# Kernel tuning notes

Measured on AMD Instinct MI355X. Metric: run time of the kernel, lower is better.

The kernel has to match this reference:

```python
import jax, jax.numpy as jnp
import numpy as np

B, S, D = 64, 1024, 128
EPS = 1e-5

def hardswish(x):
    return x * jnp.clip(x + 3.0, 0.0, 6.0) / 6.0

def setup_inputs() -> dict:
    key = jax.random.key(0)
    k1, k2, k3 = jax.random.split(key, 3)
    x = jax.random.normal(k1, (B, S, D), dtype=jnp.float32)
    ln_w = jnp.ones((S, D), dtype=jnp.float32)
    ln_b = jnp.zeros((S, D), dtype=jnp.float32)
    # U1[i]/U2[i] rows packed into lower-triangular (S,S); init ~ N(0,1)*0.01
    W1 = jax.random.normal(k2, (S, S), dtype=jnp.float32) * 0.01
    W2 = jax.random.normal(k3, (S, S), dtype=jnp.float32) * 0.01
    return {"x": x, "ln_w": ln_w, "ln_b": ln_b, "W1": W1, "W2": W2}

def reference(x, ln_w, ln_b, W1, W2):
    # LayerNorm over the last two dims (seq_len, feature_dim) jointly
    mu = jnp.mean(x, axis=(-2, -1), keepdims=True)
    var = jnp.mean(jnp.square(x - mu), axis=(-2, -1), keepdims=True)
    h = (x - mu) * jax.lax.rsqrt(var + EPS) * ln_w + ln_b
    # causal (lower-triangular) time mixing: u[:, t] = sum_{s<=t} W1[t, s] * h[:, s]
    mask = jnp.tril(jnp.ones((S, S), dtype=x.dtype))
    u = hardswish(jnp.einsum('ts,bsd->btd', W1 * mask, h))
    v = jnp.einsum('ts,bsd->btd', W2 * mask, u)
    return x + v
```

## Files before the change

### kernel.cpp

```cpp
#include <hip/hip_runtime.h>
#include <hip/hip_bf16.h>

#define NB 64
#define S_ 1024
#define D_ 128

typedef __attribute__((ext_vector_type(8))) short bf16x8;
typedef __attribute__((ext_vector_type(4))) float f32x4;
typedef __attribute__((ext_vector_type(4))) unsigned int u32x4;


__device__ __forceinline__ unsigned short f2bf(float f) {
  __hip_bfloat16 h = __float2bfloat16(f);
  return __builtin_bit_cast(unsigned short, h);
}

__device__ __forceinline__ void async_copy16(const void* g, void* l) {
  __builtin_amdgcn_global_load_lds(
      (const __attribute__((address_space(1))) unsigned int*)g,
      (__attribute__((address_space(3))) unsigned int*)l, 16, 0, 0);
}

__device__ __forceinline__ void store16_dev(void* p, bf16x8 v) {
  u32x4 d = __builtin_bit_cast(u32x4, v);
  asm volatile("global_store_dwordx4 %0, %1, off sc1" ::"v"(p), "v"(d)
               : "memory");
}

__device__ __forceinline__ void spin_mask(unsigned* p, unsigned need) {
  if (threadIdx.x == 0) {
    int guard = 0;
    while ((__hip_atomic_load(p, __ATOMIC_RELAXED, __HIP_MEMORY_SCOPE_AGENT) &
            need) != need) {
      __builtin_amdgcn_s_sleep(1);
      if (++guard > 2000000) break;
    }
  }
  __syncthreads();
  asm volatile("" ::: "memory");
}

__device__ __forceinline__ void publish_bit(unsigned* p, unsigned bit) {
  asm volatile("s_waitcnt vmcnt(0)" ::: "memory");
  __syncthreads();
  if (threadIdx.x == 0)
    __hip_atomic_fetch_or(p, bit, __ATOMIC_RELAXED, __HIP_MEMORY_SCOPE_AGENT);
}

__global__ __launch_bounds__(256) void wpack_kernel(
    const float* __restrict__ W1, const float* __restrict__ W2,
    unsigned short* __restrict__ W1f, unsigned short* __restrict__ W2f,
    unsigned* __restrict__ stats) {
  const int blk = blockIdx.x;
  const int t = threadIdx.x;
  const int wave = t >> 6, lane = t & 63;
  const int quad = lane >> 4, l16 = lane & 15;
  if (blk == 0) {
#pragma unroll
    for (int i = 0; i < 8; ++i) stats[t + i * 256] = 0u;
  }
#pragma unroll
  for (int rep = 0; rep < 2; ++rep) {
    const int u = blk * 8 + wave * 2 + rep;
    const int f = u & 2047;
    const int p = f >> 5, c = f & 31;
    const int r = p * 16 + l16;
    const int k0 = c * 32 + quad * 8;
    const float* wsrc = ((u >> 11) ? W2 : W1) + (size_t)r * 1024 + k0;
    float4 a0 = ((const float4*)wsrc)[0];
    float4 a1 = ((const float4*)wsrc)[1];
    float av[8] = {a0.x, a0.y, a0.z, a0.w, a1.x, a1.y, a1.z, a1.w};
    bf16x8 o;
#pragma unroll
    for (int jj = 0; jj < 8; ++jj)
      o[jj] = (short)f2bf((k0 + jj <= r) ? av[jj] : 0.f);
    unsigned short* dstp = ((u >> 11) ? W2f : W1f) +
                           ((size_t)p * 32 + c) * 512 + lane * 8;
    *(bf16x8*)dstp = o;
  }
}

template <bool HSWISH>
__device__ __forceinline__ void gemm_phase(
    unsigned short* ldsA, const int b, const int mt, unsigned* flags,
    const unsigned short* __restrict__ Af, const unsigned short* __restrict__ Bf,
    unsigned short* __restrict__ Uf, const float* __restrict__ Xres,
    float* __restrict__ Out) {
  const int t = threadIdx.x;
  const int wave = t >> 6, lane = t & 63;
  const int quad = lane >> 4, l16 = lane & 15;
  const int row0 = mt * 64;

  const int cend = 2 * (mt + 1);
  const int nq = (cend + 3) >> 2;

  const unsigned short* Ab = Af + (size_t)mt * 4 * 32 * 512;
  const unsigned short* Bb = Bf + (size_t)b * (D_ * S_);

  spin_mask(flags, (2u << mt) - 1);

  auto STAGE = [&](int q) {
    unsigned short* buf = ldsA + (q & 1) * 8192;
    const int c0 = q * 4;
    if (wave < cend - c0) {
#pragma unroll
      for (int jc = 0; jc < 4; ++jc) {
        const int flat16 = jc * 256 + t;
        async_copy16(Ab + ((size_t)jc * 32 + c0 + wave) * 512 + lane * 8,
                     buf + flat16 * 8);
      }
    }
  };

  STAGE(0);
  if (nq > 1) STAGE(1);
  __builtin_amdgcn_sched_barrier(0);

  f32x4 acc[4][2] = {};
  bf16x8 Bp[4][2];
#pragma unroll
  for (int g = 0; g < 4; ++g) {
    const int gg = (g < cend) ? g : 0;
#pragma unroll
    for (int jj = 0; jj < 2; ++jj)
      Bp[g][jj] = *(const bf16x8*)(Bb + ((size_t)(wave * 2 + jj) * 32 + gg) * 512 + lane * 8);
  }

  for (int q = 0; q < nq; ++q) {
    if (q < nq - 1)
      asm volatile("s_waitcnt vmcnt(12)" ::: "memory");
    else
      asm volatile("s_waitcnt vmcnt(8)" ::: "memory");
    __builtin_amdgcn_s_barrier();
    __builtin_amdgcn_sched_barrier(0);
    unsigned short* buf = ldsA + (q & 1) * 8192;
#pragma unroll
    for (int c = 0; c < 4; ++c) {
      const int g = q * 4 + c;
      if (g < cend) {
        bf16x8 af[4];
#pragma unroll
        for (int i = 0; i < 4; ++i)
          af[i] = *(const bf16x8*)(buf + i * 2048 + c * 512 + lane * 8);
        __builtin_amdgcn_s_setprio(1);
#pragma unroll
        for (int i = 0; i < 4; ++i)
#pragma unroll
          for (int jj = 0; jj < 2; ++jj)
            acc[i][jj] = __builtin_amdgcn_mfma_f32_16x16x32_bf16(
                af[i], Bp[c][jj], acc[i][jj], 0, 0, 0);
        __builtin_amdgcn_s_setprio(0);
      }
      const int gn = (g + 4 < cend) ? (g + 4) : 0;
#pragma unroll
      for (int jj = 0; jj < 2; ++jj)
        Bp[c][jj] = *(const bf16x8*)(
            Bb + ((size_t)(wave * 2 + jj) * 32 + gn) * 512 + lane * 8);
    }
    __builtin_amdgcn_sched_barrier(0);
    __builtin_amdgcn_s_barrier();
    __builtin_amdgcn_sched_barrier(0);
    if (q + 2 < nq) STAGE(q + 2);
  }

  if (HSWISH) {
    __syncthreads();
    unsigned short* ldsT = ldsA;
#pragma unroll
    for (int i = 0; i < 4; ++i)
#pragma unroll
      for (int jj = 0; jj < 2; ++jj) {
        ushort4 pk;
        float v0 = acc[i][jj][0], v1 = acc[i][jj][1], v2 = acc[i][jj][2], v3 = acc[i][jj][3];
        pk.x = f2bf(v0 * fminf(fmaxf(v0 + 3.f, 0.f), 6.f) * (1.f / 6.f));
        pk.y = f2bf(v1 * fminf(fmaxf(v1 + 3.f, 0.f), 6.f) * (1.f / 6.f));
        pk.z = f2bf(v2 * fminf(fmaxf(v2 + 3.f, 0.f), 6.f) * (1.f / 6.f));
        pk.w = f2bf(v3 * fminf(fmaxf(v3 + 3.f, 0.f), 6.f) * (1.f / 6.f));
        const int n = wave * 32 + jj * 16 + l16;
        const int m0 = i * 16 + quad * 4;
        *(ushort4*)(ldsT + n * 72 + m0) = pk;
      }
    __syncthreads();
    unsigned short* gU = Uf + (size_t)b * (D_ * S_);
#pragma unroll
    for (int ff = 0; ff < 4; ++ff) {
      const int f = wave * 4 + ff;
      const int p2 = f >> 1, cl = f & 1;
      const int d = p2 * 16 + l16;
      const int tb = cl * 32 + quad * 8;
      bf16x8 v = *(const bf16x8*)(ldsT + d * 72 + tb);
      store16_dev(gU + ((size_t)p2 * 32 + mt * 2 + cl) * 512 + lane * 8, v);
    }
  } else {
    float* gO = Out + (size_t)b * S_ * D_;
    const float* gX = Xres + (size_t)b * S_ * D_;
#pragma unroll
    for (int i = 0; i < 4; ++i) {
      const int mrow0 = row0 + i * 16 + quad * 4;
#pragma unroll
      for (int jj = 0; jj < 2; ++jj) {
        const int col = wave * 32 + jj * 16 + l16;
#pragma unroll
        for (int r = 0; r < 4; ++r) {
          const int addr = (mrow0 + r) * D_ + col;
          gO[addr] = gX[addr] + acc[i][jj][r];
        }
      }
    }
  }
}

__global__ __launch_bounds__(256, 4) void mega_kernel(
    const float* __restrict__ x, const float* __restrict__ ln_w,
    const float* __restrict__ ln_b, const unsigned short* __restrict__ W1f,
    const unsigned short* __restrict__ W2f, float* __restrict__ stats,
    unsigned short* __restrict__ hTf, unsigned short* __restrict__ uTf,
    float* __restrict__ out) {
  __shared__ __align__(16) unsigned short smem[16384];

  const int bi = blockIdx.x;
  const int xcd = bi & 7;
  const int slot = bi >> 3;
  const int b = xcd * 8 + (slot & 7);
  const int j = slot >> 3;
  const int mt = (j < 8) ? j : (j ^ 3);

  const int t = threadIdx.x;
  const int wave = t >> 6, lane = t & 63;
  const int quad = lane >> 4, l16 = lane & 15;

  float* sb = stats + (size_t)b * 32;
  unsigned* cntp = (unsigned*)sb + 2;
  unsigned* hmp = (unsigned*)sb + 4;
  unsigned* ump = (unsigned*)sb + 6;

  float2* w4 = (float2*)(smem + 8448);
  float* mr = (float*)(smem + 8464);

  const float4* xb = (const float4*)(x + ((size_t)b * S_ + mt * 64) * D_);
  {
    float s = 0.f, q = 0.f;
#pragma unroll
    for (int i = 0; i < 8; ++i) {
      float4 v = xb[i * 256 + t];
      s += v.x + v.y + v.z + v.w;
      q += v.x * v.x + v.y * v.y + v.z * v.z + v.w * v.w;
    }
#pragma unroll
    for (int o = 32; o > 0; o >>= 1) {
      s += __shfl_down(s, o, 64);
      q += __shfl_down(q, o, 64);
    }
    if (lane == 0) w4[wave] = make_float2(s, q);
  }
  __syncthreads();
  if (t == 0) {
    float ss = 0.f, qq = 0.f;
#pragma unroll
    for (int i = 0; i < 4; ++i) { ss += w4[i].x; qq += w4[i].y; }
    float o1 = __hip_atomic_fetch_add(sb + 0, ss, __ATOMIC_RELAXED,
                                      __HIP_MEMORY_SCOPE_AGENT);
    float o2 = __hip_atomic_fetch_add(sb + 1, qq, __ATOMIC_RELAXED,
                                      __HIP_MEMORY_SCOPE_AGENT);
    asm volatile("" ::"v"(o1), "v"(o2));
    __hip_atomic_fetch_add(cntp, 1u, __ATOMIC_RELAXED,
                           __HIP_MEMORY_SCOPE_AGENT);
    int guard = 0;
    while (__hip_atomic_load(cntp, __ATOMIC_RELAXED,
                             __HIP_MEMORY_SCOPE_AGENT) < 16u) {
      __builtin_amdgcn_s_sleep(1);
      if (++guard > 2000000) break;
    }
    float s1 = __hip_atomic_load(sb + 0, __ATOMIC_RELAXED,
                                 __HIP_MEMORY_SCOPE_AGENT);
    float s2 = __hip_atomic_load(sb + 1, __ATOMIC_RELAXED,
                                 __HIP_MEMORY_SCOPE_AGENT);
    const float inv = 1.0f / (S_ * D_);
    const float mu = s1 * inv;
    mr[0] = mu;
    mr[1] = rsqrtf(s2 * inv - mu * mu + 1e-5f);
  }
  __syncthreads();
  const float mu = mr[0];
  const float rs = mr[1];

  {
    unsigned short* lds = smem;
    const float4* wb = (const float4*)(ln_w + (size_t)(mt * 64) * D_);
    const float4* bv4 = (const float4*)(ln_b + (size_t)(mt * 64) * D_);
#pragma unroll
    for (int r = 0; r < 8; ++r) {
      const int f = r * 256 + t;
      const int srow = f >> 5;
      const int c4 = f & 31;
      float4 xv = xb[f];
      float4 wv = wb[f];
      float4 bvv = bv4[f];
      ushort4 o;
      o.x = f2bf((xv.x - mu) * rs * wv.x + bvv.x);
      o.y = f2bf((xv.y - mu) * rs * wv.y + bvv.y);
      o.z = f2bf((xv.z - mu) * rs * wv.z + bvv.z);
      o.w = f2bf((xv.w - mu) * rs * wv.w + bvv.w);
      *(ushort4*)(lds + srow * 132 + c4 * 4) = o;
    }
    __syncthreads();
    unsigned short* outp = hTf + (size_t)b * (D_ * S_);
    const int cg0 = mt * 2;
#pragma unroll
    for (int ff = 0; ff < 4; ++ff) {
      const int f = wave * 4 + ff;
      const int p = f >> 1, cl = f & 1;
      const int d = p * 16 + l16;
      const int sbase = cl * 32 + quad * 8;
      bf16x8 v;
#pragma unroll
      for (int jj = 0; jj < 8; ++jj)
        v[jj] = (short)lds[(sbase + jj) * 132 + d];
      store16_dev(outp + ((size_t)p * 32 + cg0 + cl) * 512 + lane * 8, v);
    }
  }
  publish_bit(hmp, 1u << mt);

  gemm_phase<true>(smem, b, mt, hmp, W1f, hTf, uTf, nullptr, nullptr);
  publish_bit(ump, 1u << mt);

  gemm_phase<false>(smem, b, mt, ump, W2f, uTf, nullptr, x, out);
}

extern "C" void kernel_launch(void* const* d_in, const int* in_sizes, int n_in,
                              void* d_out, int out_size, void* d_ws, size_t ws_size,
                              hipStream_t stream) {
  const float* x = (const float*)d_in[0];
  const float* ln_w = (const float*)d_in[1];
  const float* ln_b = (const float*)d_in[2];
  const float* W1 = (const float*)d_in[3];
  const float* W2 = (const float*)d_in[4];
  float* out = (float*)d_out;

  char* ws = (char*)d_ws;
  float* stats = (float*)ws;
  unsigned short* W1f = (unsigned short*)(ws + 16384);
  unsigned short* W2f = W1f + (size_t)S_ * S_;
  unsigned short* hTf = W2f + (size_t)S_ * S_;
  unsigned short* uTf = hTf + (size_t)NB * D_ * S_;

  wpack_kernel<<<512, 256, 0, stream>>>(W1, W2, W1f, W2f, (unsigned*)stats);
  mega_kernel<<<1024, 256, 0, stream>>>(x, ln_w, ln_b, W1f, W2f, stats,
                                        hTf, uTf, out);
}
```

Measured before the change: 131.2 us.

## Move LayerNorm statistics into prep kernel, dropping in-kernel spin barrier

LayerNorm sum and sum-of-squares reduction moves from the mega kernel into the weight-packing prep kernel. Per-batch statistics are accumulated with atomics there, and stats zeroing moves to a hipMemsetAsync. The mega kernel then reads the finished statistics directly instead of atomically accumulating and spin-waiting on a counter for all 16 tiles of a batch. This removes the inter-block spin barrier and a pass over x inside the mega kernel, at the cost of an extra memset launch and x being read once more in the prep kernel.

```diff
diff --git a/kernel.cpp b/kernel.cpp
--- a/kernel.cpp
+++ b/kernel.cpp
@@ -47,21 +47,46 @@
     __hip_atomic_fetch_or(p, bit, __ATOMIC_RELAXED, __HIP_MEMORY_SCOPE_AGENT);
 }
 
-__global__ __launch_bounds__(256) void wpack_kernel(
-    const float* __restrict__ W1, const float* __restrict__ W2,
-    unsigned short* __restrict__ W1f, unsigned short* __restrict__ W2f,
-    unsigned* __restrict__ stats) {
+__global__ __launch_bounds__(256) void prep_kernel(
+    const float* __restrict__ x, const float* __restrict__ W1,
+    const float* __restrict__ W2, float* __restrict__ stats,
+    unsigned short* __restrict__ W1f, unsigned short* __restrict__ W2f) {
+  __shared__ float2 w4[4];
   const int blk = blockIdx.x;
   const int t = threadIdx.x;
   const int wave = t >> 6, lane = t & 63;
   const int quad = lane >> 4, l16 = lane & 15;
-  if (blk == 0) {
-#pragma unroll
-    for (int i = 0; i < 8; ++i) stats[t + i * 256] = 0u;
-  }
-#pragma unroll
-  for (int rep = 0; rep < 2; ++rep) {
-    const int u = blk * 8 + wave * 2 + rep;
+
+  if (blk < 256) {
+    const int b = blk >> 2, sl = blk & 3;
+    const float4* xb =
+        (const float4*)(x + (size_t)b * (S_ * D_) + (size_t)sl * (256 * D_));
+    float s = 0.f, q = 0.f;
+#pragma unroll
+    for (int i = 0; i < 32; ++i) {
+      float4 v = xb[i * 256 + t];
+      s += v.x + v.y + v.z + v.w;
+      q += v.x * v.x + v.y * v.y + v.z * v.z + v.w * v.w;
+    }
+#pragma unroll
+    for (int o = 32; o > 0; o >>= 1) {
+      s += __shfl_down(s, o, 64);
+      q += __shfl_down(q, o, 64);
+    }
+    if (lane == 0) w4[wave] = make_float2(s, q);
+    __syncthreads();
+    if (t == 0) {
+      float ss = 0.f, qq = 0.f;
+#pragma unroll
+      for (int i = 0; i < 4; ++i) { ss += w4[i].x; qq += w4[i].y; }
+      __hip_atomic_fetch_add(stats + (size_t)b * 32 + 0, ss, __ATOMIC_RELAXED,
+                             __HIP_MEMORY_SCOPE_AGENT);
+      __hip_atomic_fetch_add(stats + (size_t)b * 32 + 1, qq, __ATOMIC_RELAXED,
+                             __HIP_MEMORY_SCOPE_AGENT);
+    }
+  }
+  {
+    const int u = blk * 4 + wave;
     const int f = u & 2047;
     const int p = f >> 5, c = f & 31;
     const int r = p * 16 + l16;
@@ -230,67 +255,21 @@
   const int quad = lane >> 4, l16 = lane & 15;
 
   float* sb = stats + (size_t)b * 32;
-  unsigned* cntp = (unsigned*)sb + 2;
   unsigned* hmp = (unsigned*)sb + 4;
   unsigned* ump = (unsigned*)sb + 6;
 
-  float2* w4 = (float2*)(smem + 8448);
-  float* mr = (float*)(smem + 8464);
-
-  const float4* xb = (const float4*)(x + ((size_t)b * S_ + mt * 64) * D_);
-  {
-    float s = 0.f, q = 0.f;
-#pragma unroll
-    for (int i = 0; i < 8; ++i) {
-      float4 v = xb[i * 256 + t];
-      s += v.x + v.y + v.z + v.w;
-      q += v.x * v.x + v.y * v.y + v.z * v.z + v.w * v.w;
-    }
-#pragma unroll
-    for (int o = 32; o > 0; o >>= 1) {
-      s += __shfl_down(s, o, 64);
-      q += __shfl_down(q, o, 64);
-    }
-    if (lane == 0) w4[wave] = make_float2(s, q);
-  }
-  __syncthreads();
-  if (t == 0) {
-    float ss = 0.f, qq = 0.f;
-#pragma unroll
-    for (int i = 0; i < 4; ++i) { ss += w4[i].x; qq += w4[i].y; }
-    float o1 = __hip_atomic_fetch_add(sb + 0, ss, __ATOMIC_RELAXED,
-                                      __HIP_MEMORY_SCOPE_AGENT);
-    float o2 = __hip_atomic_fetch_add(sb + 1, qq, __ATOMIC_RELAXED,
-                                      __HIP_MEMORY_SCOPE_AGENT);
-    asm volatile("" ::"v"(o1), "v"(o2));
-    __hip_atomic_fetch_add(cntp, 1u, __ATOMIC_RELAXED,
-                           __HIP_MEMORY_SCOPE_AGENT);
-    int guard = 0;
-    while (__hip_atomic_load(cntp, __ATOMIC_RELAXED,
-                             __HIP_MEMORY_SCOPE_AGENT) < 16u) {
-      __builtin_amdgcn_s_sleep(1);
-      if (++guard > 2000000) break;
-    }
-    float s1 = __hip_atomic_load(sb + 0, __ATOMIC_RELAXED,
-                                 __HIP_MEMORY_SCOPE_AGENT);
-    float s2 = __hip_atomic_load(sb + 1, __ATOMIC_RELAXED,
-                                 __HIP_MEMORY_SCOPE_AGENT);
-    const float inv = 1.0f / (S_ * D_);
-    const float mu = s1 * inv;
-    mr[0] = mu;
-    mr[1] = rsqrtf(s2 * inv - mu * mu + 1e-5f);
-  }
-  __syncthreads();
-  const float mu = mr[0];
-  const float rs = mr[1];
+  const float inv = 1.0f / (S_ * D_);
+  const float mu = sb[0] * inv;
+  const float rs = rsqrtf(sb[1] * inv - mu * mu + 1e-5f);
 
   {
     unsigned short* lds = smem;
+    const float4* xb = (const float4*)(x + ((size_t)b * S_ + mt * 64) * D_);
     const float4* wb = (const float4*)(ln_w + (size_t)(mt * 64) * D_);
     const float4* bv4 = (const float4*)(ln_b + (size_t)(mt * 64) * D_);
 #pragma unroll
-    for (int r = 0; r < 8; ++r) {
-      const int f = r * 256 + t;
+    for (int rr = 0; rr < 8; ++rr) {
+      const int f = rr * 256 + t;
       const int srow = f >> 5;
       const int c4 = f & 31;
       float4 xv = xb[f];
@@ -344,7 +323,8 @@
   unsigned short* hTf = W2f + (size_t)S_ * S_;
   unsigned short* uTf = hTf + (size_t)NB * D_ * S_;
 
-  wpack_kernel<<<512, 256, 0, stream>>>(W1, W2, W1f, W2f, (unsigned*)stats);
+  hipMemsetAsync(stats, 0, 8192, stream);
+  prep_kernel<<<1024, 256, 0, stream>>>(x, W1, W2, stats, W1f, W2f);
   mega_kernel<<<1024, 256, 0, stream>>>(x, ln_w, ln_b, W1f, W2f, stats,
                                         hTf, uTf, out);
 }
```

After: 133.6 us. Within noise of the previous version (+1.8%).
